# Performance work log

Hardware: AMD Instinct MI355X
Metric: run time of the kernel (lower is better)

The kernel has to match this reference:

```python
import jax, jax.numpy as jnp
import numpy as np

B, Q, L = 64, 64, 8192
KC = 51            # NarrowConv1D kernel size
HC = KC // 2 + 1   # 26 raw symmetric-half params
N = 500
KT = N + 1         # 501 transpose-conv kernel size
HT = KT // 2 + 1   # 251 raw half params

@jax.custom_vjp
def sigmoid_st(u):
    # Sigmoid forward, straight-through (identity) backward
    return jax.nn.sigmoid(u)

def _sst_fwd(u):
    return jax.nn.sigmoid(u), None

def _sst_bwd(res, g):
    return (g,)

sigmoid_st.defvjp(_sst_fwd, _sst_bwd)

def symmetric(w):
    # cat(X, X[..., :-1].flip(-1)) -> symmetric kernel of odd length
    return jnp.concatenate([w, w[..., :-1][..., ::-1]], axis=-1)

def depthwise_conv(x, k, pad):
    # x: [B, Q, L]; k: [Q, K] one kernel per channel (groups == channels)
    return jax.lax.conv_general_dilated(
        x, k[:, None, :], window_strides=(1,), padding=[(pad, pad)],
        dimension_numbers=("NCH", "OIH", "NCH"), feature_group_count=x.shape[1])

def setup_inputs() -> dict:
    key = jax.random.key(0)
    k1, k2, k3, k4 = jax.random.split(key, 4)
    return {
        "x": jax.random.normal(k1, (B, Q, L), dtype=jnp.float32),
        "conv_w_half": jax.random.normal(k2, (HC,), dtype=jnp.float32) * 0.1,
        "tc_w_half": jax.random.normal(k3, (Q, HT), dtype=jnp.float32),
        "A_raw": jax.random.normal(k4, (Q,), dtype=jnp.float32),
    }

def reference(x, conv_w_half, tc_w_half, A_raw):
    # 1) NarrowConv1D: one symmetric kernel shared across all Q channels
    kc = symmetric(conv_w_half)                       # [51]
    kc_full = jnp.broadcast_to(kc, (Q, KC))           # ChannelSame expand
    x = depthwise_conv(x, kc_full, KC // 2)           # [B,Q,L], 'same'

    # 2) softmax over spectral axis
    x = jax.nn.softmax(x, axis=-1)

    # 3) SymmetricNormConvTranspose1d: sigmoid(straight-through) + symmetric;
    #    stride-1 transpose conv with symmetric kernel == depthwise conv with
    #    padding K-1-p = N//2
    wt = sigmoid_st(tc_w_half)                        # [Q, 251] in (0,1)
    kt = symmetric(wt)                                # [Q, 501]
    x = depthwise_conv(x, kt, N // 2)                 # [B,Q,L]

    # 4) serial lattice (reflection/transmission) recursion over Q channels
    a = sigmoid_st(A_raw)                             # [Q]
    xs = jnp.transpose(x, (1, 0, 2))                  # [Q,B,L]

    def step(carry, inp):
        r, t2 = carry
        rn, aq = inp
        tn = 1.0 - rn
        s = 1.0 / (1.0 - aq * r * rn)
        r_new = r + aq * rn * t2 * s
        t2_new = aq * t2 * tn * tn * s * s
        return (r_new, t2_new), None

    init = (jnp.zeros_like(xs[0]), jnp.ones_like(xs[0]))
    (r, _), _ = jax.lax.scan(step, init, (xs, a))

    peak = wt[-1, -1]                                 # weight[-1,0,N//2] (kernel center)
    r = r / (peak * jnp.prod(a))
    return r                                          # [B, L]
```

## Files before the change

### kernel.cpp

```cpp
#include <hip/hip_runtime.h>

#define B_ 64
#define Q_ 64
#define L_ 8192
#define KCONV 51
#define HC 26
#define HT 251
#define NCH2 34
#define NCH1 6
#define TAL_CH 34

#define A51_OFF 512
#define TA_OFF  8192
#define RN_OFF  2236416

#define MAPB(s) ((((s) & ~7) | ((((s) & 7) + ((s) >> 3)) & 7)) << 4)

typedef _Float16 f16x8 __attribute__((ext_vector_type(8)));
typedef float f32x16 __attribute__((ext_vector_type(16)));
typedef unsigned int uix2 __attribute__((ext_vector_type(2)));
typedef const __attribute__((address_space(1))) void cg_void;
typedef __attribute__((address_space(3))) void lds_void3;

__device__ __forceinline__ float sigm(float v) {
    return 1.0f / (1.0f + __expf(-v));
}

__global__ __launch_bounds__(256) void k_params(const float* __restrict__ cwh,
                                                const float* __restrict__ tcw,
                                                const float* __restrict__ araw,
                                                float* __restrict__ ws) {
    const int tid = threadIdx.x;
    const int q = blockIdx.x;
    char* wsb = (char*)ws;
    if (q < Q_) {
        for (int idx = tid; idx < NCH2 * 64; idx += 256) {
            int c = idx >> 6, lane = idx & 63;
            int hi = lane >> 5, i = lane & 31;
            int mbase = 16 * c + 8 * hi - i - 6;
            f16x8 hv;
            #pragma unroll
            for (int jj = 0; jj < 8; jj++) {
                int m = mbase + jj;
                float v = 0.0f;
                if (m >= 0 && m <= 500) {
                    int hh = (m <= 250) ? m : (500 - m);
                    v = sigm(tcw[q * HT + hh]);
                }
                hv[jj] = (_Float16)v;
            }
            *(f16x8*)(wsb + TA_OFF + ((size_t)q * (NCH2 * 64) + idx) * 16) = hv;
        }
    } else {
        if (tid < Q_) ws[tid] = sigm(araw[tid]);
        for (int idx = tid; idx < NCH1 * 64; idx += 256) {
            int c = idx >> 6, lane = idx & 63;
            int hi = lane >> 5, i = lane & 31;
            int mbase = 16 * c + 8 * hi - i - 7;
            f16x8 hv;
            #pragma unroll
            for (int jj = 0; jj < 8; jj++) {
                int m = mbase + jj;
                float v = 0.0f;
                if (m >= 0 && m < KCONV) v = cwh[m < HC ? m : (KCONV - 1 - m)];
                hv[jj] = (_Float16)v;
            }
            *(f16x8*)(wsb + A51_OFF + idx * 16) = hv;
        }
        __syncthreads();
        if (tid == 0) {
            float p = 1.0f;
            for (int j = 0; j < Q_; j++) p *= ws[j];
            float peak = sigm(tcw[(Q_ - 1) * HT + 250]);
            ws[64] = 1.0f / (peak * p);
        }
    }
}

__device__ __forceinline__ void write_dlayout(char* buf, int base_slot,
                                              const float* v, float scale,
                                              int w, int j, int hi) {
    union P4 { _Float16 h[4]; uint2 u; };
    P4 p[4];
    #pragma unroll
    for (int k = 0; k < 4; k++) {
        #pragma unroll
        for (int d = 0; d < 4; d++) p[k].h[d] = (_Float16)(v[4 * k + d] * scale);
    }
#if __has_builtin(__builtin_amdgcn_permlane32_swap)
    uix2 s0x = __builtin_amdgcn_permlane32_swap(p[0].u.x, p[2].u.x, false, false);
    uix2 s0y = __builtin_amdgcn_permlane32_swap(p[0].u.y, p[2].u.y, false, false);
    uix2 s1x = __builtin_amdgcn_permlane32_swap(p[1].u.x, p[3].u.x, false, false);
    uix2 s1y = __builtin_amdgcn_permlane32_swap(p[1].u.y, p[3].u.y, false, false);
    uint4 w0, w1;
    if (hi == 0) {
        w0.x = p[0].u.x; w0.y = p[0].u.y; w0.z = s0x[1]; w0.w = s0y[1];
        w1.x = p[1].u.x; w1.y = p[1].u.y; w1.z = s1x[1]; w1.w = s1y[1];
    } else {
        w0.x = s0x[0]; w0.y = s0y[0]; w0.z = p[2].u.x; w0.w = p[2].u.y;
        w1.x = s1x[0]; w1.y = s1y[0]; w1.z = p[3].u.x; w1.w = p[3].u.y;
    }
    const int s0 = base_slot + 128 * w + 4 * j + 2 * hi;
    *(uint4*)(buf + MAPB(s0)) = w0;
    *(uint4*)(buf + MAPB(s0 + 1)) = w1;
#else
    #pragma unroll
    for (int k = 0; k < 4; k++) {
        const int bo = MAPB(base_slot + 128 * w + 4 * j + k) + 8 * hi;
        *(uint2*)(buf + bo) = p[k].u;
    }
#endif
}

__global__ __launch_bounds__(512, 4) void k_fused(const float* __restrict__ x,
                                                  float* __restrict__ ws) {
    const int tid = threadIdx.x;
    const int bid = blockIdx.x;
    const int q = bid >> 5, pr = bid & 31;
    const int row0 = (2 * pr) * Q_ + q, row1 = (2 * pr + 1) * Q_ + q;
    char* wsb = (char*)ws;
    __shared__ __attribute__((aligned(128))) char bufA[17408];
    __shared__ __attribute__((aligned(128))) char bufB[17408];
    __shared__ __attribute__((aligned(128))) char TAL[TAL_CH * 1024];
    __shared__ float red[32];

    const int w = tid >> 6, lane = tid & 63, j = lane & 31, hi = lane >> 5;

    {
        const char* tabg = wsb + TA_OFF + (size_t)q * (NCH2 * 64) * 16;
        for (int c = w; c < TAL_CH; c += 8) {
            const void* gp = tabg + (c * 64 + lane) * 16;
            __builtin_amdgcn_global_load_lds((cg_void*)gp,
                                             (lds_void3*)(TAL + c * 1024), 16, 0, 0);
        }
    }

    f16x8 a51r[NCH1];
    #pragma unroll
    for (int c = 0; c < NCH1; c++)
        a51r[c] = *(const f16x8*)(wsb + A51_OFF + (c * 64 + lane) * 16);

    const uint4 z4 = {0u, 0u, 0u, 0u};
    if (tid < 32) {
        *(uint4*)(bufA + MAPB(tid)) = z4;
        *(uint4*)(bufB + MAPB(tid)) = z4;
    } else if (tid >= 64 && tid < 96) {
        int s = 1056 + (tid - 64);
        *(uint4*)(bufA + MAPB(s)) = z4;
        *(uint4*)(bufB + MAPB(s)) = z4;
    }

    union H8 { _Float16 h[8]; uint4 u; };
    {
        #pragma unroll
        for (int r = 0; r < 2; r++) {
            const float* xr = x + (size_t)(r ? row1 : row0) * L_ + 16 * tid;
            char* buf = r ? bufB : bufA;
            float4 f0 = *(const float4*)(xr + 0);
            float4 f1 = *(const float4*)(xr + 4);
            float4 f2 = *(const float4*)(xr + 8);
            float4 f3 = *(const float4*)(xr + 12);
            H8 h0, h1;
            h0.h[0] = (_Float16)f0.x; h0.h[1] = (_Float16)f0.y;
            h0.h[2] = (_Float16)f0.z; h0.h[3] = (_Float16)f0.w;
            h0.h[4] = (_Float16)f1.x; h0.h[5] = (_Float16)f1.y;
            h0.h[6] = (_Float16)f1.z; h0.h[7] = (_Float16)f1.w;
            h1.h[0] = (_Float16)f2.x; h1.h[1] = (_Float16)f2.y;
            h1.h[2] = (_Float16)f2.z; h1.h[3] = (_Float16)f2.w;
            h1.h[4] = (_Float16)f3.x; h1.h[5] = (_Float16)f3.y;
            h1.h[6] = (_Float16)f3.z; h1.h[7] = (_Float16)f3.w;
            *(uint4*)(buf + MAPB(2 * tid + 32)) = h0.u;
            *(uint4*)(buf + MAPB(2 * tid + 33)) = h1.u;
        }
    }
    __syncthreads();

    f32x16 acc0 = {}, acc1 = {};
    {
        f16x8 pA[2], pB[2];
        pA[0] = *(const f16x8*)(bufA + MAPB(128 * w + 4 * j + 28 + hi));
        pB[0] = *(const f16x8*)(bufB + MAPB(128 * w + 4 * j + 28 + hi));
        pA[1] = *(const f16x8*)(bufA + MAPB(128 * w + 4 * j + 30 + hi));
        pB[1] = *(const f16x8*)(bufB + MAPB(128 * w + 4 * j + 30 + hi));
        #pragma unroll
        for (int c = 0; c < NCH1; c++) {
            acc0 = __builtin_amdgcn_mfma_f32_32x32x16_f16(a51r[c], pA[c & 1], acc0, 0, 0, 0);
            acc1 = __builtin_amdgcn_mfma_f32_32x32x16_f16(a51r[c], pB[c & 1], acc1, 0, 0, 0);
            if (c + 2 < NCH1) {
                const int bo = MAPB(128 * w + 4 * j + 2 * (c + 2) + 28 + hi);
                pA[c & 1] = *(const f16x8*)(bufA + bo);
                pB[c & 1] = *(const f16x8*)(bufB + bo);
            }
        }
    }

    float mx0 = -3.402823466e+38f, mx1 = -3.402823466e+38f;
    #pragma unroll
    for (int e = 0; e < 16; e++) { mx0 = fmaxf(mx0, acc0[e]); mx1 = fmaxf(mx1, acc1[e]); }
    #pragma unroll
    for (int o = 32; o > 0; o >>= 1) {
        mx0 = fmaxf(mx0, __shfl_xor(mx0, o));
        mx1 = fmaxf(mx1, __shfl_xor(mx1, o));
    }
    float sm0 = 0.0f, sm1 = 0.0f;
    #pragma unroll
    for (int e = 0; e < 16; e++) {
        acc0[e] = __expf(acc0[e] - mx0); sm0 += acc0[e];
        acc1[e] = __expf(acc1[e] - mx1); sm1 += acc1[e];
    }
    #pragma unroll
    for (int o = 32; o > 0; o >>= 1) { sm0 += __shfl_xor(sm0, o); sm1 += __shfl_xor(sm1, o); }
    if (lane == 0) {
        red[w] = mx0; red[8 + w] = sm0;
        red[16 + w] = mx1; red[24 + w] = sm1;
    }
    __syncthreads();
    float mg0 = red[0], mg1 = red[16];
    #pragma unroll
    for (int i = 1; i < 8; i++) { mg0 = fmaxf(mg0, red[i]); mg1 = fmaxf(mg1, red[16 + i]); }
    float ss0 = 0.0f, ss1 = 0.0f;
    #pragma unroll
    for (int i = 0; i < 8; i++) {
        ss0 += red[8 + i] * __expf(red[i] - mg0);
        ss1 += red[24 + i] * __expf(red[16 + i] - mg1);
    }
    const float isum0 = __expf(mx0 - mg0) / ss0;
    const float isum1 = __expf(mx1 - mg1) / ss1;

    write_dlayout(bufA, 32, (const float*)&acc0, isum0, w, j, hi);
    write_dlayout(bufB, 32, (const float*)&acc1, isum1, w, j, hi);
    __syncthreads();

    f32x16 o0 = {}, o1 = {};
    {
        f16x8 afr[4], pA[2], pB[2];
        #pragma unroll
        for (int c = 0; c < 4; c++)
            afr[c] = *(const f16x8*)(TAL + c * 1024 + lane * 16);
        #pragma unroll
        for (int c = 0; c < 2; c++) {
            const int bo = MAPB(128 * w + 4 * j + 2 * c + hi);
            pA[c] = *(const f16x8*)(bufA + bo);
            pB[c] = *(const f16x8*)(bufB + bo);
        }
        #pragma unroll
        for (int c = 0; c < NCH2; c++) {
            o0 = __builtin_amdgcn_mfma_f32_32x32x16_f16(afr[c & 3], pA[c & 1], o0, 0, 0, 0);
            o1 = __builtin_amdgcn_mfma_f32_32x32x16_f16(afr[c & 3], pB[c & 1], o1, 0, 0, 0);
            if (c + 2 < NCH2) {
                const int bo = MAPB(128 * w + 4 * j + 2 * (c + 2) + hi);
                pA[c & 1] = *(const f16x8*)(bufA + bo);
                pB[c & 1] = *(const f16x8*)(bufB + bo);
            }
            if (c + 4 < NCH2)
                afr[c & 3] = *(const f16x8*)(TAL + (c + 4) * 1024 + lane * 16);
        }
    }
    __syncthreads();

    write_dlayout(bufA, 0, (const float*)&o0, 1.0f, w, j, hi);
    write_dlayout(bufB, 0, (const float*)&o1, 1.0f, w, j, hi);
    __syncthreads();
    {
        uint4 r0 = *(uint4*)(bufA + MAPB(2 * tid));
        uint4 r1 = *(uint4*)(bufA + MAPB(2 * tid + 1));
        char* dst = wsb + RN_OFF + ((size_t)row0 * L_ + 16 * tid) * 2;
        *(uint4*)dst = r0;
        *(uint4*)(dst + 16) = r1;
        uint4 r2 = *(uint4*)(bufB + MAPB(2 * tid));
        uint4 r3 = *(uint4*)(bufB + MAPB(2 * tid + 1));
        char* dst1 = wsb + RN_OFF + ((size_t)row1 * L_ + 16 * tid) * 2;
        *(uint4*)dst1 = r2;
        *(uint4*)(dst1 + 16) = r3;
    }
}

__global__ __launch_bounds__(256) void k_lat(const float* __restrict__ ws,
                                             float* __restrict__ out) {
    const int tid = threadIdx.x;
    const int T = blockIdx.x & 7, b = blockIdx.x >> 3;
    const char* wsb = (const char*)ws;
    const int l = 1024 * T + 4 * tid;
    const char* src = wsb + RN_OFF + ((size_t)(b * Q_) * L_ + l) * 2;
    float r[4] = {0.0f, 0.0f, 0.0f, 0.0f};
    float t2[4] = {1.0f, 1.0f, 1.0f, 1.0f};
    union P4 { _Float16 h[4]; uint2 u; };
    P4 cur;
    cur.u = *(const uint2*)src;
    for (int q = 0; q < Q_; q++) {
        P4 nxt = cur;
        if (q < Q_ - 1) nxt.u = *(const uint2*)(src + (size_t)(q + 1) * L_ * 2);
        const float aq = ws[q];
        #pragma unroll
        for (int e = 0; e < 4; e++) {
            float rn = (float)cur.h[e], tn = 1.0f - rn;
            float si = 1.0f / (1.0f - aq * r[e] * rn);
            float rnew = r[e] + aq * rn * t2[e] * si;
            t2[e] = aq * t2[e] * tn * tn * si * si;
            r[e] = rnew;
        }
        cur = nxt;
    }
    const float inv_scale = ws[64];
    float4 o;
    o.x = r[0] * inv_scale; o.y = r[1] * inv_scale;
    o.z = r[2] * inv_scale; o.w = r[3] * inv_scale;
    *(float4*)&out[(size_t)b * L_ + l] = o;
}

extern "C" void kernel_launch(void* const* d_in, const int* in_sizes, int n_in,
                              void* d_out, int out_size, void* d_ws, size_t ws_size,
                              hipStream_t stream) {
    (void)in_sizes; (void)n_in; (void)out_size; (void)ws_size;
    const float* x    = (const float*)d_in[0];
    const float* cwh  = (const float*)d_in[1];
    const float* tcw  = (const float*)d_in[2];
    const float* araw = (const float*)d_in[3];
    float* out = (float*)d_out;
    float* ws  = (float*)d_ws;

    hipLaunchKernelGGL(k_params, dim3(Q_ + 1), dim3(256), 0, stream, cwh, tcw, araw, ws);
    hipLaunchKernelGGL(k_fused, dim3((B_ / 2) * Q_), dim3(512), 0, stream, x, ws);
    hipLaunchKernelGGL(k_lat, dim3(B_ * 8), dim3(256), 0, stream, ws, out);
}
```

Baseline: 96.44 us.

## Store conv output in MFMA-native permuted layout, skip LDS transpose

The transpose-conv epilogue no longer stages accumulators through LDS with two barriers to build a linear row layout. Each lane converts its MFMA accumulators to fp16 and writes them straight to the workspace in a permuted layout. The lattice kernel reads that permuted layout directly and remaps the output index so results land in the correct spectral positions. This removes LDS round-trips and syncs, but the global stores may be less coalesced and the index remapping must match the MFMA output ordering exactly.

```diff
diff --git a/kernel.cpp b/kernel.cpp
--- a/kernel.cpp
+++ b/kernel.cpp
@@ -256,22 +256,26 @@
                 afr[c & 3] = *(const f16x8*)(TAL + (c + 4) * 1024 + lane * 16);
         }
     }
-    __syncthreads();
-
-    write_dlayout(bufA, 0, (const float*)&o0, 1.0f, w, j, hi);
-    write_dlayout(bufB, 0, (const float*)&o1, 1.0f, w, j, hi);
-    __syncthreads();
-    {
-        uint4 r0 = *(uint4*)(bufA + MAPB(2 * tid));
-        uint4 r1 = *(uint4*)(bufA + MAPB(2 * tid + 1));
-        char* dst = wsb + RN_OFF + ((size_t)row0 * L_ + 16 * tid) * 2;
-        *(uint4*)dst = r0;
-        *(uint4*)(dst + 16) = r1;
-        uint4 r2 = *(uint4*)(bufB + MAPB(2 * tid));
-        uint4 r3 = *(uint4*)(bufB + MAPB(2 * tid + 1));
-        char* dst1 = wsb + RN_OFF + ((size_t)row1 * L_ + 16 * tid) * 2;
-        *(uint4*)dst1 = r2;
-        *(uint4*)(dst1 + 16) = r3;
+
+    {
+        union P4 { _Float16 h[4]; uint2 u; };
+        const int lofs = w * 2048 + (2 * j + hi) * 32;
+        #pragma unroll
+        for (int r = 0; r < 2; r++) {
+            const float* v = r ? (const float*)&o1 : (const float*)&o0;
+            P4 p[4];
+            #pragma unroll
+            for (int k = 0; k < 4; k++) {
+                #pragma unroll
+                for (int d = 0; d < 4; d++) p[k].h[d] = (_Float16)v[4 * k + d];
+            }
+            uint4 w0, w1;
+            w0.x = p[0].u.x; w0.y = p[0].u.y; w0.z = p[1].u.x; w0.w = p[1].u.y;
+            w1.x = p[2].u.x; w1.y = p[2].u.y; w1.z = p[3].u.x; w1.w = p[3].u.y;
+            char* dst = wsb + RN_OFF + (size_t)(r ? row1 : row0) * 16384 + lofs;
+            *(uint4*)dst = w0;
+            *(uint4*)(dst + 16) = w1;
+        }
     }
 }
 
@@ -280,8 +284,7 @@
     const int tid = threadIdx.x;
     const int T = blockIdx.x & 7, b = blockIdx.x >> 3;
     const char* wsb = (const char*)ws;
-    const int l = 1024 * T + 4 * tid;
-    const char* src = wsb + RN_OFF + ((size_t)(b * Q_) * L_ + l) * 2;
+    const char* src = wsb + RN_OFF + (size_t)(b * Q_) * 16384 + T * 2048 + tid * 8;
     float r[4] = {0.0f, 0.0f, 0.0f, 0.0f};
     float t2[4] = {1.0f, 1.0f, 1.0f, 1.0f};
     union P4 { _Float16 h[4]; uint2 u; };
@@ -289,7 +292,7 @@
     cur.u = *(const uint2*)src;
     for (int q = 0; q < Q_; q++) {
         P4 nxt = cur;
-        if (q < Q_ - 1) nxt.u = *(const uint2*)(src + (size_t)(q + 1) * L_ * 2);
+        if (q < Q_ - 1) nxt.u = *(const uint2*)(src + (size_t)(q + 1) * 16384);
         const float aq = ws[q];
         #pragma unroll
         for (int e = 0; e < 4; e++) {
@@ -302,6 +305,7 @@
         cur = nxt;
     }
     const float inv_scale = ws[64];
+    const int l = 1024 * T + 32 * (tid >> 3) + 8 * (tid & 3) + 4 * ((tid >> 2) & 1);
     float4 o;
     o.x = r[0] * inv_scale; o.y = r[1] * inv_scale;
     o.z = r[2] * inv_scale; o.w = r[3] * inv_scale;
```

Result: no change. 94.55 us (-2.0%).
